# Performance work log

Measured on AMD Instinct MI355X. Metric: run time of the kernel, lower is better.

Reference implementation:

```python
import jax, jax.numpy as jnp
import numpy as np

HIDDEN = 1280
NUM_HEADS = 16
HEAD_DIM = HIDDEN // NUM_HEADS  # 80
ROPE_DIM = HEAD_DIM // 2        # 40
THETA = 10000.0
SEQ = 3072


def setup_inputs() -> dict:
    key = jax.random.key(0)
    ks = jax.random.split(key, 6)
    hidden_states = jax.random.normal(ks[0], (SEQ, HIDDEN), dtype=jnp.float32)
    position_ids = jax.random.randint(ks[1], (SEQ, 2), 0, 64, dtype=jnp.int32)
    qkv_w = jax.random.normal(ks[2], (HIDDEN, 3 * HIDDEN), dtype=jnp.float32) * (HIDDEN ** -0.5)
    qkv_b = jax.random.normal(ks[3], (3 * HIDDEN,), dtype=jnp.float32) * 0.02
    o_w = jax.random.normal(ks[4], (HIDDEN, HIDDEN), dtype=jnp.float32) * (HIDDEN ** -0.5)
    o_b = jax.random.normal(ks[5], (HIDDEN,), dtype=jnp.float32) * 0.02
    return {"hidden_states": hidden_states, "position_ids": position_ids,
            "qkv_w": qkv_w, "qkv_b": qkv_b, "o_w": o_w, "o_b": o_b}


def _rotate_half(x):
    x1, x2 = jnp.split(x, 2, axis=-1)
    return jnp.concatenate([-x2, x1], axis=-1)


def reference(hidden_states, position_ids, qkv_w, qkv_b, o_w, o_b):
    seq_len = hidden_states.shape[0]
    # fused QKV projection
    qkv = hidden_states @ qkv_w + qkv_b                     # (S, 3*H*D)
    qkv = qkv.reshape(seq_len, 3, NUM_HEADS, HEAD_DIM)
    q, k, v = qkv[:, 0], qkv[:, 1], qkv[:, 2]               # each (S, h, d)
    # 2D RoPE: inv_freq over rope dim = head_dim // 2
    inv_freq = 1.0 / (THETA ** (jnp.arange(0, ROPE_DIM, 2, dtype=jnp.float32) / ROPE_DIM))
    pos = position_ids.astype(jnp.float32)
    h_freqs = jnp.outer(pos[:, 0], inv_freq)                # (S, rope/2)
    w_freqs = jnp.outer(pos[:, 1], inv_freq)                # (S, rope/2)
    freqs = jnp.concatenate([h_freqs, w_freqs], axis=-1)    # (S, rope)
    emb = jnp.concatenate([freqs, freqs], axis=-1)          # (S, head_dim)
    cos = jnp.cos(emb)[:, None, :]                          # (S, 1, d)
    sin = jnp.sin(emb)[:, None, :]
    q = q * cos + _rotate_half(q) * sin
    k = k * cos + _rotate_half(k) * sin
    # manual attention
    scaling = HEAD_DIM ** -0.5
    attn = jnp.einsum('qhd,khd->hqk', q * scaling, k)       # (h, S, S)
    attn = jax.nn.softmax(attn, axis=-1)
    out = jnp.einsum('hqk,khd->qhd', attn, v)               # (S, h, d)
    out = out.reshape(seq_len, HIDDEN)
    return out @ o_w + o_b
```

## Files before the change

kernel.cpp:

```cpp
#include <hip/hip_runtime.h>

#define SEQ  3072
#define HID  1280
#define NH   16
#define HD   80
#define NQKV 3840
#define KSP  2

typedef unsigned short u16;
typedef unsigned int u32;
typedef __attribute__((ext_vector_type(8))) short short8;
typedef __attribute__((ext_vector_type(4))) short short4v;
typedef __attribute__((ext_vector_type(4))) float floatx4;
typedef __attribute__((ext_vector_type(4))) unsigned int uint4v;

__device__ __forceinline__ u16 f2bf(float x) {
    u32 u = __float_as_uint(x);
    u += 0x7fffu + ((u >> 16) & 1u);
    return (u16)(u >> 16);
}
__device__ __forceinline__ u32 packrne(float a, float b) {
    return (u32)f2bf(a) | ((u32)f2bf(b) << 16);
}

typedef const __attribute__((address_space(1))) unsigned int* gp1_t;
typedef __attribute__((address_space(3))) unsigned int* lp3_t;
__device__ __forceinline__ void gld16(const void* g, void* l) {
    __builtin_amdgcn_global_load_lds((gp1_t)g, (lp3_t)l, 16, 0, 0);
}

__device__ __forceinline__ int swz80(int c, int r) {
    return (c < 8) ? (c ^ (r & 7)) : (8 + ((c - 8) ^ ((r >> 2) & 1)));
}

__global__ void prep_k(const int* __restrict__ pos, float2* __restrict__ csb,
                       const float* __restrict__ hs,
                       u16* __restrict__ hH, const float* __restrict__ qkvw,
                       u16* __restrict__ wT, const float* __restrict__ ow,
                       u16* __restrict__ owT) {
    __shared__ float tile[32][33];
    const int b = blockIdx.x, t = threadIdx.x;
    if (b < 480) {
        int i = b * 256 + t;
        int s = i / 40, j = i % 40;
        float p = (float)((j < 20) ? pos[s * 2] : pos[s * 2 + 1]);
        int k = (j < 20) ? j : j - 20;
        float inv = powf(10000.0f, -(float)k / 20.0f);
        float a = p * inv;
        csb[s * 40 + j] = make_float2(cosf(a), sinf(a));
    } else if (b < 4320) {
        int i = (b - 480) * 256 + t;
        const float4 x = ((const float4*)hs)[i];
        uint2 o;
        o.x = packrne(x.x, x.y);
        o.y = packrne(x.z, x.w);
        ((uint2*)hH)[i] = o;
    } else {
        const float* w;
        u16* dst;
        int K, N, nx, ky;
        if (b < 9120) {
            int i = b - 4320;
            nx = i % 120; ky = i / 120; w = qkvw; dst = wT; K = HID; N = NQKV;
        } else {
            int i = b - 9120;
            nx = i % 40; ky = i / 40; w = ow; dst = owT; K = HID; N = HID;
        }
        int n0 = nx * 32, k0 = ky * 32;
        int c = t & 31, r8 = t >> 5;
        for (int rr = r8; rr < 32; rr += 8)
            tile[rr][c] = w[(size_t)(k0 + rr) * N + n0 + c];
        __syncthreads();
        for (int rr = r8; rr < 32; rr += 8)
            dst[(size_t)(n0 + rr) * K + k0 + c] = f2bf(tile[c][rr]);
    }
}

__global__ __launch_bounds__(256, 4) void gemm_qkv_k(
    const u16* __restrict__ A, const u16* __restrict__ B,
    const float* __restrict__ bias, const float2* __restrict__ csb,
    u16* __restrict__ Qs, u16* __restrict__ Ks, u16* __restrict__ Vs) {
    __shared__ u16 lA[128 * 64], lB[80 * 64];
    const int t = threadIdx.x, lane = t & 63, w = t >> 6;
    const int qi = lane & 15, quad = lane >> 4;
    const int K = HID;
    int id = blockIdx.x;
    int xcd = id & 7, sN = id >> 3;
    int m_idx = (xcd >> 1) * 6 + sN / 24;
    int n_idx = (xcd & 1) * 24 + sN % 24;
    const int m0 = m_idx * 128;
    const int nb = n_idx * 80;

    floatx4 acc[2][5];
    for (int mi = 0; mi < 2; mi++)
        for (int ni = 0; ni < 5; ni++) acc[mi][ni] = (floatx4){0.f, 0.f, 0.f, 0.f};

    const int rg = lane >> 3;
    const int ce = ((lane & 7) ^ rg) * 8;
    size_t gA[4];
    for (int j = 0; j < 4; j++) {
        int row = m0 + (w * 4 + j) * 8 + rg;
        gA[j] = (size_t)row * K + ce;
    }
    size_t gB[3];
    int nB = 0;
    for (int g = w; g < 10; g += 4) {
        int row = nb + g * 8 + rg;
        gB[nB++] = (size_t)row * K + ce;
    }

    for (int k0 = 0; k0 < K; k0 += 64) {
        for (int j = 0; j < 4; j++)
            gld16(A + gA[j] + k0, &lA[((w * 4 + j) * 8) * 64]);
        {
            int bi = 0;
            for (int g = w; g < 10; g += 4)
                gld16(B + gB[bi++] + k0, &lB[(g * 8) * 64]);
        }
        __syncthreads();
        short8 af[2][2];
        for (int mi = 0; mi < 2; mi++) {
            int row = w * 32 + mi * 16 + qi;
            for (int kh = 0; kh < 2; kh++)
                af[mi][kh] = *(const short8*)&lA[row * 64 + (((kh * 4 + quad) ^ (row & 7)) << 3)];
        }
#pragma unroll
        for (int ni = 0; ni < 5; ni++) {
            int row = ni * 16 + qi;
            short8 b0 = *(const short8*)&lB[row * 64 + ((quad ^ (row & 7)) << 3)];
            short8 b1 = *(const short8*)&lB[row * 64 + (((4 + quad) ^ (row & 7)) << 3)];
            for (int mi = 0; mi < 2; mi++) {
                acc[mi][ni] = __builtin_amdgcn_mfma_f32_16x16x32_bf16(af[mi][0], b0, acc[mi][ni], 0, 0, 0);
                acc[mi][ni] = __builtin_amdgcn_mfma_f32_16x16x32_bf16(af[mi][1], b1, acc[mi][ni], 0, 0, 0);
            }
        }
        __syncthreads();
    }

    const int ht = n_idx >> 4;
    const int h = n_idx & 15;
    float bs[5];
    for (int ni = 0; ni < 5; ni++)
        bs[ni] = bias[ht * HID + h * HD + ni * 16 + qi];

    if (ht == 2) {
        for (int mi = 0; mi < 2; mi++) {
            int s = m0 + w * 32 + mi * 16 + quad * 4;
            int g = (s & 63) >> 2;
            size_t base = (size_t)(s & ~63);
            for (int ni = 0; ni < 5; ni++) {
                int d = ni * 16 + qi;
                uint2 o;
                o.x = packrne(acc[mi][ni][0] + bs[ni], acc[mi][ni][1] + bs[ni]);
                o.y = packrne(acc[mi][ni][2] + bs[ni], acc[mi][ni][3] + bs[ni]);
                int pc = (g >> 1) ^ (d & 7);
                *(uint2*)&Vs[((size_t)h * HD + d) * SEQ + base + pc * 8 + (g & 1) * 4] = o;
            }
        }
    } else {
        const float qsc = (ht == 0) ? 0.11180339887498949f * 1.4426950408889634f : 1.0f;
        u16* dst = (ht == 0) ? Qs : Ks;
        int dm[5];
        dm[0] = qi;
        dm[1] = 16 + qi;
        dm[2] = (qi & 8) ? (qi - 8) : (32 + qi);
        dm[3] = 8 + qi;
        dm[4] = 24 + qi;
        for (int mi = 0; mi < 2; mi++) {
#pragma unroll
            for (int r = 0; r < 4; r++) {
                int s = m0 + w * 32 + mi * 16 + quad * 4 + r;
                float val[5], sh[5];
                for (int ni = 0; ni < 5; ni++) val[ni] = acc[mi][ni][r] + bs[ni];
                for (int ni = 0; ni < 5; ni++) sh[ni] = __shfl_xor(val[ni], 8);
                const float2* cr = csb + (size_t)s * 40;
                float out[5];
                {
                    float2 c0 = cr[dm[0]];
                    float p = (qi & 8) ? sh[3] : sh[2];
                    out[0] = (val[0] * c0.x - p * c0.y) * qsc;
                    float2 c1 = cr[dm[1]];
                    p = (qi & 8) ? sh[4] : sh[3];
                    out[1] = (val[1] * c1.x - p * c1.y) * qsc;
                    float2 c2 = cr[dm[2]];
                    if (qi & 8) out[2] = (val[2] * c2.x + sh[0] * c2.y) * qsc;
                    else        out[2] = (val[2] * c2.x - sh[4] * c2.y) * qsc;
                    float2 c3 = cr[dm[3]];
                    p = (qi & 8) ? sh[1] : sh[0];
                    out[3] = (val[3] * c3.x + p * c3.y) * qsc;
                    float2 c4 = cr[dm[4]];
                    p = (qi & 8) ? sh[2] : sh[1];
                    out[4] = (val[4] * c4.x + p * c4.y) * qsc;
                }
                size_t rowb = (size_t)(h * SEQ + s) * 80;
                for (int ni = 0; ni < 5; ni++) {
                    int c = 2 * ni + (qi >> 3);
                    dst[rowb + swz80(c, s) * 8 + (qi & 7)] = f2bf(out[ni]);
                }
            }
        }
    }
}

template<int BM, int BN>
__global__ __launch_bounds__(256, 3) void gemm_bf16_k(
    const u16* __restrict__ A, const u16* __restrict__ B,
    const float* __restrict__ bias, float* __restrict__ C,
    int M, int N, int K, int mode) {
    constexpr int GA = BM / 32;
    constexpr int GB = BN / 32;
    constexpr int FM = BM / 32;
    constexpr int FN = BN / 32;
    __shared__ u16 lA[BM * 64], lB[BN * 64];
    const int t = threadIdx.x, lane = t & 63, w = t >> 6;
    const int qi = lane & 15, quad = lane >> 4;
    int id = blockIdx.x;
    int xcd = id & 7, sN = id >> 3;
    int m_idx, n_idx;
    if (mode == 0) {
        n_idx = (xcd & 1) * 15 + sN % 15;
        m_idx = (xcd >> 1) * 6 + sN / 15;
    } else {
        m_idx = xcd * 6 + sN / 20;
        n_idx = sN % 20;
    }
    const int m0 = m_idx * BM, n0 = n_idx * BN;
    const int wm = (w >> 1) * (BM / 2), wn = (w & 1) * (BN / 2);

    floatx4 acc[FM][FN];
    for (int mi = 0; mi < FM; mi++)
        for (int ni = 0; ni < FN; ni++) acc[mi][ni] = (floatx4){0.f, 0.f, 0.f, 0.f};

    const int rg = lane >> 3;
    const int ce = ((lane & 7) ^ rg) * 8;
    size_t gA[GA], gB[GB];
    for (int g = 0; g < GA; g++) {
        int row = w * (BM / 4) + g * 8 + rg;
        gA[g] = (size_t)(m0 + row) * K + ce;
    }
    for (int g = 0; g < GB; g++) {
        int row = w * (BN / 4) + g * 8 + rg;
        gB[g] = (size_t)(n0 + row) * K + ce;
    }

    for (int k0 = 0; k0 < K; k0 += 64) {
        for (int g = 0; g < GA; g++)
            gld16(A + gA[g] + k0, &lA[(w * (BM / 4) + g * 8) * 64]);
        for (int g = 0; g < GB; g++)
            gld16(B + gB[g] + k0, &lB[(w * (BN / 4) + g * 8) * 64]);
        __syncthreads();
        short8 af[FM][2], bf[FN][2];
        for (int mi = 0; mi < FM; mi++) {
            int row = wm + mi * 16 + qi;
            for (int kh = 0; kh < 2; kh++)
                af[mi][kh] = *(const short8*)&lA[row * 64 + (((kh * 4 + quad) ^ (row & 7)) << 3)];
        }
        for (int ni = 0; ni < FN; ni++) {
            int row = wn + ni * 16 + qi;
            for (int kh = 0; kh < 2; kh++)
                bf[ni][kh] = *(const short8*)&lB[row * 64 + (((kh * 4 + quad) ^ (row & 7)) << 3)];
        }
        for (int mi = 0; mi < FM; mi++)
            for (int ni = 0; ni < FN; ni++) {
                acc[mi][ni] = __builtin_amdgcn_mfma_f32_16x16x32_bf16(af[mi][0], bf[ni][0], acc[mi][ni], 0, 0, 0);
                acc[mi][ni] = __builtin_amdgcn_mfma_f32_16x16x32_bf16(af[mi][1], bf[ni][1], acc[mi][ni], 0, 0, 0);
            }
        __syncthreads();
    }
    for (int mi = 0; mi < FM; mi++)
        for (int ni = 0; ni < FN; ni++) {
            int col = n0 + wn + ni * 16 + qi;
            int rowb = m0 + wm + mi * 16 + quad * 4;
            float b = bias[col];
            for (int r = 0; r < 4; r++)
                C[(size_t)(rowb + r) * N + col] = acc[mi][ni][r] + b;
        }
}

__global__ __launch_bounds__(512, 6) void attn_k(
    const u16* __restrict__ Qs, const u16* __restrict__ Ks, const u16* __restrict__ Vs,
    float* __restrict__ Op, float* __restrict__ lp) {
    __shared__ u16 kbuf[2][5120];
    __shared__ u16 vbuf[2][5120];

    const int t = threadIdx.x, lane = t & 63, w = t >> 6;
    const int qi = lane & 15, quad = lane >> 4;
    const int h = blockIdx.y, q0 = blockIdx.x * 128, ksp = blockIdx.z;
    const int kc0 = ksp * (SEQ / 2);
    u16* const kflat = &kbuf[0][0];

    {
        const u16* Qt = Qs + (size_t)(h * SEQ + q0) * 80;
        for (int i = w; i < 20; i += 8)
            gld16(Qt + i * 512 + lane * 8, kflat + i * 512);
    }
    __syncthreads();
    short8 bq[3];
    {
        const u16* rb = &kflat[(w * 16 + qi) * 80];
        bq[0] = *(const short8*)&rb[(quad ^ (qi & 7)) << 3];
        bq[1] = *(const short8*)&rb[((4 + quad) ^ (qi & 7)) << 3];
        short4v t2 = *(const short4v*)&rb[((8 + ((quad >> 1) ^ ((qi >> 2) & 1))) << 3) + ((quad & 1) << 2)];
        bq[2] = (short8){t2.x, t2.y, t2.z, t2.w, 0, 0, 0, 0};
    }
    __syncthreads();

    float l_lane = 0.f;
    floatx4 acco[5];
    for (int dt = 0; dt < 5; dt++) acco[dt] = (floatx4){0.f, 0.f, 0.f, 0.f};

    auto stage = [&](int it, int buf) {
        int kc = kc0 + it * 64;
        const u16* Kt = Ks + (size_t)(h * SEQ + kc) * 80;
        for (int i = w; i < 10; i += 8)
            gld16(Kt + i * 512 + lane * 8, &kbuf[buf][i * 512]);
        const u16* Vt = Vs + (size_t)h * HD * SEQ + kc;
        for (int i = w; i < 10; i += 8) {
            int p16 = i * 64 + lane;
            int d = p16 >> 3, pc = p16 & 7;
            gld16(Vt + (size_t)d * SEQ + pc * 8, &vbuf[buf][i * 512]);
        }
    };
    stage(0, 0);
    __syncthreads();

    const int NT = (SEQ / 2) / 64;
    for (int it = 0; it < NT; it++) {
        int cur = it & 1;
        if (it + 1 < NT) stage(it + 1, cur ^ 1);
        const u16* kb = &kbuf[cur][0];
        const u16* vb = &vbuf[cur][0];
#pragma unroll
        for (int c2 = 0; c2 < 2; c2++) {
            u32 pkx[2], pky[2];
#pragma unroll
            for (int ktl = 0; ktl < 2; ktl++) {
                int arow = (c2 * 2 + ktl) * 16 + qi;
                const u16* rb = &kb[arow * 80];
                short8 a0 = *(const short8*)&rb[(quad ^ (qi & 7)) << 3];
                short8 a1 = *(const short8*)&rb[((4 + quad) ^ (qi & 7)) << 3];
                short4v a2v = *(const short4v*)&rb[((8 + ((quad >> 1) ^ ((qi >> 2) & 1))) << 3) + ((quad & 1) << 2)];
                short8 a2 = (short8){a2v.x, a2v.y, a2v.z, a2v.w, 0, 0, 0, 0};
                floatx4 s = (floatx4){0.f, 0.f, 0.f, 0.f};
                __builtin_amdgcn_s_setprio(1);
                s = __builtin_amdgcn_mfma_f32_16x16x32_bf16(a0, bq[0], s, 0, 0, 0);
                s = __builtin_amdgcn_mfma_f32_16x16x32_bf16(a1, bq[1], s, 0, 0, 0);
                s = __builtin_amdgcn_mfma_f32_16x16x32_bf16(a2, bq[2], s, 0, 0, 0);
                __builtin_amdgcn_s_setprio(0);
                float e0 = __builtin_amdgcn_exp2f(s[0]);
                float e1 = __builtin_amdgcn_exp2f(s[1]);
                float e2 = __builtin_amdgcn_exp2f(s[2]);
                float e3 = __builtin_amdgcn_exp2f(s[3]);
                l_lane += (e0 + e1) + (e2 + e3);
                pkx[ktl] = __builtin_amdgcn_perm(__float_as_uint(e1), __float_as_uint(e0), 0x07060302u);
                pky[ktl] = __builtin_amdgcn_perm(__float_as_uint(e3), __float_as_uint(e2), 0x07060302u);
            }
            auto s0 = __builtin_amdgcn_permlane32_swap(pkx[0], pkx[1], false, false);
            auto s1 = __builtin_amdgcn_permlane32_swap(pky[0], pky[1], false, false);
            auto t0 = __builtin_amdgcn_permlane16_swap(s0[0], s0[1], false, false);
            auto t1 = __builtin_amdgcn_permlane16_swap(s1[0], s1[1], false, false);
            uint4v bb = (uint4v){t0[0], t1[0], t0[1], t1[1]};
            short8 bp = __builtin_bit_cast(short8, bb);
            int pv = (4 * c2 + quad) ^ (qi & 7);
            __builtin_amdgcn_s_setprio(1);
#pragma unroll
            for (int dt = 0; dt < 5; dt++) {
                short8 av = *(const short8*)&vb[((dt * 16 + qi) * 8 + pv) * 8];
                acco[dt] = __builtin_amdgcn_mfma_f32_16x16x32_bf16(av, bp, acco[dt], 0, 0, 0);
            }
            __builtin_amdgcn_s_setprio(0);
        }
        __syncthreads();
    }

    {
        float lq = l_lane;
        lq += __shfl_xor(lq, 16);
        lq += __shfl_xor(lq, 32);
        int q = q0 + w * 16 + qi;
        if (quad == 0) lp[(size_t)(ksp * NH + h) * SEQ + q] = lq;
        for (int dt = 0; dt < 5; dt++)
            for (int r = 0; r < 4; r++) {
                int d = dt * 16 + quad * 4 + r;
                Op[((size_t)(ksp * NH + h) * HD + d) * SEQ + q] = acco[dt][r];
            }
    }
}

__global__ void merge_k(const float* __restrict__ Op, const float* __restrict__ lp,
                        u16* __restrict__ att) {
    __shared__ float ls[HD * 65];
    __shared__ float li[64];
    const int t = threadIdx.x;
    const int h = blockIdx.y, q0 = blockIdx.x * 64;
    for (int i = t; i < HD * 16; i += 256) {
        int d = i / 16, g = i % 16;
        size_t a0 = ((size_t)h * HD + d) * SEQ + q0 + g * 4;
        size_t a1 = ((size_t)(NH + h) * HD + d) * SEQ + q0 + g * 4;
        const float4 v0 = *(const float4*)&Op[a0];
        const float4 v1 = *(const float4*)&Op[a1];
        ls[d * 65 + g * 4 + 0] = v0.x + v1.x;
        ls[d * 65 + g * 4 + 1] = v0.y + v1.y;
        ls[d * 65 + g * 4 + 2] = v0.z + v1.z;
        ls[d * 65 + g * 4 + 3] = v0.w + v1.w;
    }
    if (t < 64)
        li[t] = 1.0f / (lp[(size_t)h * SEQ + q0 + t] + lp[(size_t)(NH + h) * SEQ + q0 + t]);
    __syncthreads();
    for (int i = t; i < 64 * 40; i += 256) {
        int ql = i / 40, dg = i % 40;
        int d0 = dg * 2;
        float s = li[ql];
        u32 o = packrne(ls[d0 * 65 + ql] * s, ls[(d0 + 1) * 65 + ql] * s);
        *(u32*)&att[(size_t)(q0 + ql) * HID + h * HD + d0] = o;
    }
}

extern "C" void kernel_launch(void* const* d_in, const int* in_sizes, int n_in,
                              void* d_out, int out_size, void* d_ws, size_t ws_size,
                              hipStream_t stream) {
    const float* hs   = (const float*)d_in[0];
    const int*   pos  = (const int*)d_in[1];
    const float* qkvw = (const float*)d_in[2];
    const float* qkvb = (const float*)d_in[3];
    const float* ow   = (const float*)d_in[4];
    const float* ob   = (const float*)d_in[5];
    float* out = (float*)d_out;

    char* p = (char*)d_ws;
    auto alloc = [&](size_t bytes) {
        char* r = p;
        p += (bytes + 255) & ~(size_t)255;
        return r;
    };
    float2* csb = (float2*)alloc((size_t)SEQ * 40 * 8);
    u16* owT = (u16*)alloc((size_t)HID * HID * 2);
    u16* hH  = (u16*)alloc((size_t)SEQ * HID * 2);
    u16* Qs  = (u16*)alloc((size_t)NH * SEQ * HD * 2);
    u16* Ks  = (u16*)alloc((size_t)NH * SEQ * HD * 2);
    u16* Vs  = (u16*)alloc((size_t)NH * SEQ * HD * 2);
    char* poolB = alloc((size_t)KSP * NH * HD * SEQ * 4);
    u16* wT = (u16*)poolB;
    float* Op = (float*)poolB;
    float* lp = (float*)alloc((size_t)KSP * NH * SEQ * 4);
    u16* att = hH;

    hipLaunchKernelGGL(prep_k, dim3(10720), dim3(256), 0, stream,
                       pos, csb, hs, hH, qkvw, wT, ow, owT);
    hipLaunchKernelGGL(gemm_qkv_k, dim3(1152), dim3(256), 0, stream,
                       hH, wT, qkvb, csb, Qs, Ks, Vs);
    hipLaunchKernelGGL(attn_k, dim3(SEQ / 128, NH, 2), dim3(512), 0, stream,
                       Qs, Ks, Vs, Op, lp);
    hipLaunchKernelGGL(merge_k, dim3(SEQ / 64, NH), dim3(256), 0, stream, Op, lp, att);
    hipLaunchKernelGGL((gemm_bf16_k<64, 64>), dim3(960), dim3(256), 0, stream,
                       att, owT, ob, out, SEQ, HID, HID, 1);
}
```

Before: 227.4 us.

## Process two query groups per wave in attention to reuse K/V LDS reads

The attention kernel now uses 256 threads per block, and each wave handles 32 query rows (two 16-row groups) instead of 16. Each K fragment and V fragment read from LDS therefore feeds twice as many MFMAs. K/V staging is redistributed so each wave issues five loads, and the two-barrier-per-iteration sync is replaced by a partial vmcnt wait plus a single raw s_barrier. The trade is higher register pressure (doubled accumulators and Q fragments), fewer waves per block, and reliance on hand-placed waitcnt for correct double buffering.

After: 228.0 us. No clear change (+0.3%).

```diff
diff --git a/kernel.cpp b/kernel.cpp
--- a/kernel.cpp
+++ b/kernel.cpp
@@ -277,7 +277,7 @@
         }
 }
 
-__global__ __launch_bounds__(512, 6) void attn_k(
+__global__ __launch_bounds__(256, 3) void attn_k(
     const u16* __restrict__ Qs, const u16* __restrict__ Ks, const u16* __restrict__ Vs,
     float* __restrict__ Op, float* __restrict__ lp) {
     __shared__ u16 kbuf[2][5120];
@@ -291,48 +291,62 @@
 
     {
         const u16* Qt = Qs + (size_t)(h * SEQ + q0) * 80;
-        for (int i = w; i < 20; i += 8)
-            gld16(Qt + i * 512 + lane * 8, kflat + i * 512);
+        for (int j = 0; j < 5; j++) {
+            int o = (w * 5 + j) * 512;
+            gld16(Qt + o + lane * 8, kflat + o);
+        }
     }
     __syncthreads();
-    short8 bq[3];
-    {
-        const u16* rb = &kflat[(w * 16 + qi) * 80];
-        bq[0] = *(const short8*)&rb[(quad ^ (qi & 7)) << 3];
-        bq[1] = *(const short8*)&rb[((4 + quad) ^ (qi & 7)) << 3];
+    short8 bq[2][3];
+    for (int qg = 0; qg < 2; qg++) {
+        const u16* rb = &kflat[(w * 32 + qg * 16 + qi) * 80];
+        bq[qg][0] = *(const short8*)&rb[(quad ^ (qi & 7)) << 3];
+        bq[qg][1] = *(const short8*)&rb[((4 + quad) ^ (qi & 7)) << 3];
         short4v t2 = *(const short4v*)&rb[((8 + ((quad >> 1) ^ ((qi >> 2) & 1))) << 3) + ((quad & 1) << 2)];
-        bq[2] = (short8){t2.x, t2.y, t2.z, t2.w, 0, 0, 0, 0};
+        bq[qg][2] = (short8){t2.x, t2.y, t2.z, t2.w, 0, 0, 0, 0};
     }
     __syncthreads();
 
-    float l_lane = 0.f;
-    floatx4 acco[5];
-    for (int dt = 0; dt < 5; dt++) acco[dt] = (floatx4){0.f, 0.f, 0.f, 0.f};
-
+    float l_lane[2] = {0.f, 0.f};
+    floatx4 acco[2][5];
+    for (int qg = 0; qg < 2; qg++)
+        for (int dt = 0; dt < 5; dt++) acco[qg][dt] = (floatx4){0.f, 0.f, 0.f, 0.f};
+
+    const u16* const Kt = Ks + (size_t)(h * SEQ + kc0) * 80;
+    const u16* const Vt = Vs + (size_t)h * HD * SEQ + kc0;
     auto stage = [&](int it, int buf) {
-        int kc = kc0 + it * 64;
-        const u16* Kt = Ks + (size_t)(h * SEQ + kc) * 80;
-        for (int i = w; i < 10; i += 8)
-            gld16(Kt + i * 512 + lane * 8, &kbuf[buf][i * 512]);
-        const u16* Vt = Vs + (size_t)h * HD * SEQ + kc;
-        for (int i = w; i < 10; i += 8) {
-            int p16 = i * 64 + lane;
-            int d = p16 >> 3, pc = p16 & 7;
-            gld16(Vt + (size_t)d * SEQ + pc * 8, &vbuf[buf][i * 512]);
+        const u16* Kti = Kt + it * (64 * 80);
+        const u16* Vti = Vt + it * 64;
+        for (int c = 0; c < 5; c++) {
+            int j = w * 5 + c;
+            if (j < 10) {
+                gld16(Kti + j * 512 + lane * 8, &kbuf[buf][j * 512]);
+            } else {
+                int i = j - 10;
+                int p16 = i * 64 + lane;
+                int d = p16 >> 3, pc = p16 & 7;
+                gld16(Vti + (size_t)d * SEQ + pc * 8, &vbuf[buf][i * 512]);
+            }
         }
     };
     stage(0, 0);
-    __syncthreads();
 
     const int NT = (SEQ / 2) / 64;
     for (int it = 0; it < NT; it++) {
         int cur = it & 1;
-        if (it + 1 < NT) stage(it + 1, cur ^ 1);
+        if (it + 1 < NT) {
+            stage(it + 1, cur ^ 1);
+            asm volatile("s_waitcnt vmcnt(5)" ::: "memory");
+        } else {
+            asm volatile("s_waitcnt vmcnt(0)" ::: "memory");
+        }
+        __builtin_amdgcn_s_barrier();
+        __builtin_amdgcn_sched_barrier(0);
         const u16* kb = &kbuf[cur][0];
         const u16* vb = &vbuf[cur][0];
 #pragma unroll
         for (int c2 = 0; c2 < 2; c2++) {
-            u32 pkx[2], pky[2];
+            u32 pkx[2][2], pky[2][2];
 #pragma unroll
             for (int ktl = 0; ktl < 2; ktl++) {
                 int arow = (c2 * 2 + ktl) * 16 + qi;
@@ -341,48 +355,56 @@
                 short8 a1 = *(const short8*)&rb[((4 + quad) ^ (qi & 7)) << 3];
                 short4v a2v = *(const short4v*)&rb[((8 + ((quad >> 1) ^ ((qi >> 2) & 1))) << 3) + ((quad & 1) << 2)];
                 short8 a2 = (short8){a2v.x, a2v.y, a2v.z, a2v.w, 0, 0, 0, 0};
-                floatx4 s = (floatx4){0.f, 0.f, 0.f, 0.f};
-                __builtin_amdgcn_s_setprio(1);
-                s = __builtin_amdgcn_mfma_f32_16x16x32_bf16(a0, bq[0], s, 0, 0, 0);
-                s = __builtin_amdgcn_mfma_f32_16x16x32_bf16(a1, bq[1], s, 0, 0, 0);
-                s = __builtin_amdgcn_mfma_f32_16x16x32_bf16(a2, bq[2], s, 0, 0, 0);
-                __builtin_amdgcn_s_setprio(0);
-                float e0 = __builtin_amdgcn_exp2f(s[0]);
-                float e1 = __builtin_amdgcn_exp2f(s[1]);
-                float e2 = __builtin_amdgcn_exp2f(s[2]);
-                float e3 = __builtin_amdgcn_exp2f(s[3]);
-                l_lane += (e0 + e1) + (e2 + e3);
-                pkx[ktl] = __builtin_amdgcn_perm(__float_as_uint(e1), __float_as_uint(e0), 0x07060302u);
-                pky[ktl] = __builtin_amdgcn_perm(__float_as_uint(e3), __float_as_uint(e2), 0x07060302u);
-            }
-            auto s0 = __builtin_amdgcn_permlane32_swap(pkx[0], pkx[1], false, false);
-            auto s1 = __builtin_amdgcn_permlane32_swap(pky[0], pky[1], false, false);
-            auto t0 = __builtin_amdgcn_permlane16_swap(s0[0], s0[1], false, false);
-            auto t1 = __builtin_amdgcn_permlane16_swap(s1[0], s1[1], false, false);
-            uint4v bb = (uint4v){t0[0], t1[0], t0[1], t1[1]};
-            short8 bp = __builtin_bit_cast(short8, bb);
+#pragma unroll
+                for (int qg = 0; qg < 2; qg++) {
+                    floatx4 s = (floatx4){0.f, 0.f, 0.f, 0.f};
+                    __builtin_amdgcn_s_setprio(1);
+                    s = __builtin_amdgcn_mfma_f32_16x16x32_bf16(a0, bq[qg][0], s, 0, 0, 0);
+                    s = __builtin_amdgcn_mfma_f32_16x16x32_bf16(a1, bq[qg][1], s, 0, 0, 0);
+                    s = __builtin_amdgcn_mfma_f32_16x16x32_bf16(a2, bq[qg][2], s, 0, 0, 0);
+                    __builtin_amdgcn_s_setprio(0);
+                    float e0 = __builtin_amdgcn_exp2f(s[0]);
+                    float e1 = __builtin_amdgcn_exp2f(s[1]);
+                    float e2 = __builtin_amdgcn_exp2f(s[2]);
+                    float e3 = __builtin_amdgcn_exp2f(s[3]);
+                    l_lane[qg] += (e0 + e1) + (e2 + e3);
+                    pkx[qg][ktl] = __builtin_amdgcn_perm(__float_as_uint(e1), __float_as_uint(e0), 0x07060302u);
+                    pky[qg][ktl] = __builtin_amdgcn_perm(__float_as_uint(e3), __float_as_uint(e2), 0x07060302u);
+                }
+            }
+            short8 bp[2];
+#pragma unroll
+            for (int qg = 0; qg < 2; qg++) {
+                auto s0 = __builtin_amdgcn_permlane32_swap(pkx[qg][0], pkx[qg][1], false, false);
+                auto s1 = __builtin_amdgcn_permlane32_swap(pky[qg][0], pky[qg][1], false, false);
+                auto t0 = __builtin_amdgcn_permlane16_swap(s0[0], s0[1], false, false);
+                auto t1 = __builtin_amdgcn_permlane16_swap(s1[0], s1[1], false, false);
+                uint4v bb = (uint4v){t0[0], t1[0], t0[1], t1[1]};
+                bp[qg] = __builtin_bit_cast(short8, bb);
+            }
             int pv = (4 * c2 + quad) ^ (qi & 7);
             __builtin_amdgcn_s_setprio(1);
 #pragma unroll
             for (int dt = 0; dt < 5; dt++) {
                 short8 av = *(const short8*)&vb[((dt * 16 + qi) * 8 + pv) * 8];
-                acco[dt] = __builtin_amdgcn_mfma_f32_16x16x32_bf16(av, bp, acco[dt], 0, 0, 0);
+                acco[0][dt] = __builtin_amdgcn_mfma_f32_16x16x32_bf16(av, bp[0], acco[0][dt], 0, 0, 0);
+                acco[1][dt] = __builtin_amdgcn_mfma_f32_16x16x32_bf16(av, bp[1], acco[1][dt], 0, 0, 0);
             }
             __builtin_amdgcn_s_setprio(0);
         }
-        __syncthreads();
-    }
-
-    {
-        float lq = l_lane;
+        __builtin_amdgcn_s_barrier();
+    }
+
+    for (int qg = 0; qg < 2; qg++) {
+        float lq = l_lane[qg];
         lq += __shfl_xor(lq, 16);
         lq += __shfl_xor(lq, 32);
-        int q = q0 + w * 16 + qi;
+        int q = q0 + w * 32 + qg * 16 + qi;
         if (quad == 0) lp[(size_t)(ksp * NH + h) * SEQ + q] = lq;
         for (int dt = 0; dt < 5; dt++)
             for (int r = 0; r < 4; r++) {
                 int d = dt * 16 + quad * 4 + r;
-                Op[((size_t)(ksp * NH + h) * HD + d) * SEQ + q] = acco[dt][r];
+                Op[((size_t)(ksp * NH + h) * HD + d) * SEQ + q] = acco[qg][dt][r];
             }
     }
 }
@@ -449,7 +471,7 @@
                        pos, csb, hs, hH, qkvw, wT, ow, owT);
     hipLaunchKernelGGL(gemm_qkv_k, dim3(1152), dim3(256), 0, stream,
                        hH, wT, qkvb, csb, Qs, Ks, Vs);
-    hipLaunchKernelGGL(attn_k, dim3(SEQ / 128, NH, 2), dim3(512), 0, stream,
+    hipLaunchKernelGGL(attn_k, dim3(SEQ / 128, NH, 2), dim3(256), 0, stream,
                        Qs, Ks, Vs, Op, lp);
     hipLaunchKernelGGL(merge_k, dim3(SEQ / 64, NH), dim3(256), 0, stream, Op, lp, att);
     hipLaunchKernelGGL((gemm_bf16_k<64, 64>), dim3(960), dim3(256), 0, stream,
```
